# Performance work log

Hardware: AMD Instinct MI355X
Metric: run time of the kernel (lower is better)

The kernel has to match this reference:

```python
import jax, jax.numpy as jnp
import numpy as np

H = 4096        # hidden_size
NH = 32         # num query heads
NKV = 8         # num kv heads
D = H // NH     # head_dim = 128
S = 2048        # num tokens (single causal sequence)
THETA = 1000000.0
SCALE = D ** -0.5


def _rope(x, positions):
    # neox-style (rotate-half) RoPE over full head_dim, as vLLM's get_rope default
    half = D // 2
    inv_freq = 1.0 / (THETA ** (jnp.arange(half, dtype=jnp.float32) / half))
    ang = positions.astype(jnp.float32)[:, None] * inv_freq          # [S, D/2]
    cos = jnp.cos(ang)[:, None, :]                                   # [S, 1, D/2]
    sin = jnp.sin(ang)[:, None, :]
    x1, x2 = x[..., :half], x[..., half:]
    return jnp.concatenate([x1 * cos - x2 * sin, x2 * cos + x1 * sin], axis=-1)


def setup_inputs() -> dict:
    key = jax.random.key(0)
    k1, k2, k3 = jax.random.split(key, 3)
    positions = jnp.arange(S, dtype=jnp.int32)
    hidden_states = jax.random.normal(k1, (S, H), dtype=jnp.float32)
    w_qkv = jax.random.normal(k2, ((NH + 2 * NKV) * D, H), dtype=jnp.float32) * 0.02
    w_o = jax.random.normal(k3, (H, NH * D), dtype=jnp.float32) * 0.02
    return {"positions": positions, "hidden_states": hidden_states,
            "w_qkv": w_qkv, "w_o": w_o}


def reference(positions, hidden_states, w_qkv, w_o):
    # fused QKV projection (Linear, bias=False): x @ W^T
    qkv = hidden_states @ w_qkv.T                                    # [S, (NH+2*NKV)*D]
    q, k, v = jnp.split(qkv, [NH * D, (NH + NKV) * D], axis=-1)
    q = q.reshape(S, NH, D)
    k = k.reshape(S, NKV, D)
    v = v.reshape(S, NKV, D)
    # RoPE on q and k
    q = _rope(q, positions)
    k = _rope(k, positions)
    # GQA causal attention: group NH query heads onto NKV kv heads
    g = NH // NKV
    qg = q.reshape(S, NKV, g, D)
    scores = jnp.einsum('qhgd,khd->hgqk', qg, k) * SCALE             # [NKV, g, S, S]
    causal = positions[:, None] >= positions[None, :]                # [S, S]
    scores = jnp.where(causal[None, None], scores, jnp.float32(-1e30))
    probs = jax.nn.softmax(scores, axis=-1)
    o = jnp.einsum('hgqk,khd->qhgd', probs, v).reshape(S, NH * D)
    return o @ w_o.T                                                 # [S, H]
```

## Files before the change

kernel.cpp:

```cpp
#include <hip/hip_runtime.h>
#include <hip/hip_bf16.h>

#define S_LEN 2048
#define HID 4096
#define NH 32
#define NKV 8
#define DH 128
#define QKV_N ((NH + 2 * NKV) * DH)
#define SCALE_ATT 0.08838834764831845f
#define SCALE2_ATT 0.12751744f

typedef __bf16 bf16;
typedef __bf16 bf16x8 __attribute__((ext_vector_type(8)));
typedef __bf16 bf16x4 __attribute__((ext_vector_type(4)));
typedef float f32x4 __attribute__((ext_vector_type(4)));
typedef float f32x16 __attribute__((ext_vector_type(16)));

__device__ inline f32x4 mfma16(bf16x8 a, bf16x8 b, f32x4 c) {
    return __builtin_amdgcn_mfma_f32_16x16x32_bf16(a, b, c, 0, 0, 0);
}
__device__ inline f32x16 mfma32(bf16x8 a, bf16x8 b, f32x16 c) {
    return __builtin_amdgcn_mfma_f32_32x32x16_bf16(a, b, c, 0, 0, 0);
}

__device__ inline bf16x8 load8(const float* p) {
    const float4 a = ((const float4*)p)[0];
    const float4 b = ((const float4*)p)[1];
    bf16x8 r;
    r[0] = (bf16)a.x; r[1] = (bf16)a.y; r[2] = (bf16)a.z; r[3] = (bf16)a.w;
    r[4] = (bf16)b.x; r[5] = (bf16)b.y; r[6] = (bf16)b.z; r[7] = (bf16)b.w;
    return r;
}
__device__ inline bf16x8 load8(const bf16* p) { return *(const bf16x8*)p; }

__device__ inline void load_lds16(const bf16* g, bf16* lds_base) {
    __builtin_amdgcn_global_load_lds(
        (const __attribute__((address_space(1))) void*)g,
        (__attribute__((address_space(3))) void*)lds_base, 16, 0, 0);
}

__device__ inline unsigned pack2_bf16(float lo, float hi) {
    union { bf16 h[2]; unsigned u; } r;
    r.h[0] = (bf16)lo;
    r.h[1] = (bf16)hi;
    return r.u;
}

__global__ __launch_bounds__(256) void cvt3_kernel(const float* __restrict__ s0, bf16* __restrict__ d0, int c0,
                                                   const float* __restrict__ s1, bf16* __restrict__ d1, int c1,
                                                   const float* __restrict__ s2, bf16* __restrict__ d2, int c2) {
    int i = blockIdx.x * 256 + threadIdx.x;
    if (i < c0) { *(bf16x8*)&d0[(size_t)i * 8] = load8(&s0[(size_t)i * 8]); return; }
    i -= c0;
    if (i < c1) { *(bf16x8*)&d1[(size_t)i * 8] = load8(&s1[(size_t)i * 8]); return; }
    i -= c1;
    if (i < c2) { *(bf16x8*)&d2[(size_t)i * 8] = load8(&s2[(size_t)i * 8]); }
}

template <int BN, typename OutT>
__global__ __launch_bounds__(512, 2) void gemm_8ph(const bf16* __restrict__ A,
                                                   const bf16* __restrict__ B,
                                                   OutT* __restrict__ C,
                                                   int K, int lda, int ldc) {
    constexpr int WTN = BN / 4;
    constexpr int NREP = WTN / 32;
    extern __shared__ char smem[];
    bf16* As = (bf16*)smem;
    bf16* Bs = (bf16*)(smem + 2 * 256 * 64 * 2);

    const int tid = threadIdx.x;
    const int lane = tid & 63;
    const int w = tid >> 6;
    const int wm = w >> 2;
    const int wn = w & 3;
    const int ln = lane & 31;
    const int hi = lane >> 5;
    const int rseg = lane >> 3;
    const int gc = (lane & 7) ^ rseg;

    const int m0 = (int)blockIdx.y * 256;
    const int n0 = (int)blockIdx.x * BN;
    const int NT = K >> 6;

    auto stageA = [&](int pb, int kt, int h) {
        const int k0 = kt * 64;
        const int rb = h * 128 + w * 16;
        const bf16* src = &A[(size_t)(m0 + rb + rseg) * lda + k0 + gc * 8];
        bf16* dst = &As[pb * (256 * 64) + rb * 64];
        load_lds16(src, dst);
        load_lds16(src + (size_t)8 * lda, dst + 8 * 64);
    };
    auto stageB = [&](int pb, int kt, int h) {
        const int k0 = kt * 64;
        if constexpr (BN == 256) {
            const int rb = h * 128 + w * 16;
            const bf16* src = &B[(size_t)(n0 + rb + rseg) * K + k0 + gc * 8];
            bf16* dst = &Bs[pb * (BN * 64) + rb * 64];
            load_lds16(src, dst);
            load_lds16(src + (size_t)8 * K, dst + 8 * 64);
        } else {
            const int rb = h * 64 + w * 8;
            const bf16* src = &B[(size_t)(n0 + rb + rseg) * K + k0 + gc * 8];
            bf16* dst = &Bs[pb * (BN * 64) + rb * 64];
            load_lds16(src, dst);
        }
    };

    f32x16 acc[4][NREP];
#pragma unroll
    for (int mi = 0; mi < 4; ++mi)
#pragma unroll
        for (int j = 0; j < NREP; ++j)
#pragma unroll
            for (int r = 0; r < 16; ++r) acc[mi][j][r] = 0.f;

    stageB(0, 0, 0); stageB(0, 0, 1);
    stageA(0, 0, 0); stageA(0, 0, 1);
    {
        const int k1 = NT > 1 ? 1 : 0;
        stageB(1, k1, 0); stageB(1, k1, 1);
    }
    if constexpr (BN == 256)
        asm volatile("s_waitcnt vmcnt(4)" ::: "memory");
    else
        asm volatile("s_waitcnt vmcnt(2)" ::: "memory");
    __builtin_amdgcn_s_barrier();

    int p = 0;
    for (int u = 0; u < NT; ++u, p ^= 1) {
        const bf16* Ab = &As[p * (256 * 64)];
        const bf16* Bb = &Bs[p * (BN * 64)];
        const int ktA = u + 1 < NT ? u + 1 : NT - 1;
        const int ktB = u + 2 < NT ? u + 2 : NT - 1;
        bf16x8 bfr[NREP][4];
#pragma unroll
        for (int q = 0; q < 4; ++q) {
            if (q == 0) {
#pragma unroll
                for (int j = 0; j < NREP; ++j)
#pragma unroll
                    for (int kk = 0; kk < 4; ++kk) {
                        const int n = wn * WTN + j * 32 + ln;
                        bfr[j][kk] = *(const bf16x8*)&Bb[n * 64 + (((2 * kk + hi) ^ (ln & 7)) * 8)];
                    }
            }
            bf16x8 af[4];
#pragma unroll
            for (int kk = 0; kk < 4; ++kk) {
                const int m = wm * 128 + q * 32 + ln;
                af[kk] = *(const bf16x8*)&Ab[m * 64 + (((2 * kk + hi) ^ (ln & 7)) * 8)];
            }
            if (q == 0) stageA(p ^ 1, ktA, 0);
            else if (q == 1) stageA(p ^ 1, ktA, 1);
            else if (q == 2) stageB(p, ktB, 0);
            else stageB(p, ktB, 1);

            __builtin_amdgcn_s_barrier();
            asm volatile("s_waitcnt lgkmcnt(0)" ::: "memory");
            __builtin_amdgcn_sched_barrier(0);
            __builtin_amdgcn_s_setprio(1);
#pragma unroll
            for (int j = 0; j < NREP; ++j)
#pragma unroll
                for (int kk = 0; kk < 4; ++kk)
                    acc[q][j] = mfma32(af[kk], bfr[j][kk], acc[q][j]);
            __builtin_amdgcn_s_setprio(0);
            __builtin_amdgcn_sched_barrier(0);
            if (q == 3) {
                if constexpr (BN == 256)
                    asm volatile("s_waitcnt vmcnt(4)" ::: "memory");
                else
                    asm volatile("s_waitcnt vmcnt(2)" ::: "memory");
            }
            __builtin_amdgcn_s_barrier();
        }
    }
    asm volatile("s_waitcnt vmcnt(0)" ::: "memory");

#pragma unroll
    for (int mi = 0; mi < 4; ++mi)
#pragma unroll
        for (int j = 0; j < NREP; ++j)
#pragma unroll
            for (int r = 0; r < 16; ++r) {
                int row = m0 + wm * 128 + mi * 32 + (r & 3) + 8 * (r >> 2) + 4 * hi;
                int col = n0 + wn * WTN + j * 32 + ln;
                C[(size_t)row * ldc + col] = (OutT)acc[mi][j][r];
            }
}

template <typename AT, typename OutT>
__global__ __launch_bounds__(256) void gemm_bt(const AT* __restrict__ A,
                                               const float* __restrict__ B,
                                               OutT* __restrict__ C,
                                               int K, int lda, int ldc) {
    const int tid = threadIdx.x;
    const int lane = tid & 63;
    const int w = tid >> 6;
    const int m0 = blockIdx.y * 128;
    const int n0 = blockIdx.x * 128;
    const int wm = (w >> 1) * 64;
    const int wn = (w & 1) * 64;
    const int ln = lane & 15;
    const int qo = lane >> 4;

    __shared__ bf16 As[128 * 72];
    __shared__ bf16 Bs[128 * 72];

    f32x4 acc[4][4];
#pragma unroll
    for (int mi = 0; mi < 4; ++mi)
#pragma unroll
        for (int ni = 0; ni < 4; ++ni) acc[mi][ni] = f32x4{0.f, 0.f, 0.f, 0.f};

    for (int k0 = 0; k0 < K; k0 += 64) {
#pragma unroll
        for (int i = 0; i < 4; ++i) {
            int v = tid + i * 256;
            int row = v >> 3;
            int col = (v & 7) * 8;
            *(bf16x8*)&As[row * 72 + col] = load8(&A[(size_t)(m0 + row) * lda + k0 + col]);
            *(bf16x8*)&Bs[row * 72 + col] = load8(&B[(size_t)(n0 + row) * K + k0 + col]);
        }
        __syncthreads();
#pragma unroll
        for (int kk = 0; kk < 64; kk += 32) {
            bf16x8 af[4], bfr[4];
#pragma unroll
            for (int mi = 0; mi < 4; ++mi)
                af[mi] = *(const bf16x8*)&As[(wm + mi * 16 + ln) * 72 + kk + qo * 8];
#pragma unroll
            for (int ni = 0; ni < 4; ++ni)
                bfr[ni] = *(const bf16x8*)&Bs[(wn + ni * 16 + ln) * 72 + kk + qo * 8];
#pragma unroll
            for (int mi = 0; mi < 4; ++mi)
#pragma unroll
                for (int ni = 0; ni < 4; ++ni)
                    acc[mi][ni] = mfma16(af[mi], bfr[ni], acc[mi][ni]);
        }
        __syncthreads();
    }
#pragma unroll
    for (int mi = 0; mi < 4; ++mi)
#pragma unroll
        for (int ni = 0; ni < 4; ++ni)
#pragma unroll
            for (int r = 0; r < 4; ++r) {
                int row = m0 + wm + mi * 16 + qo * 4 + r;
                int col = n0 + wn + ni * 16 + ln;
                C[(size_t)row * ldc + col] = (OutT)acc[mi][ni][r];
            }
}

__global__ __launch_bounds__(256) void rope_kernel(bf16* __restrict__ qkv,
                                                   const int* __restrict__ positions) {
    int idx = blockIdx.x * 256 + threadIdx.x;
    const int total = S_LEN * (NH + NKV) * 64;
    if (idx >= total) return;
    int d = idx & 63;
    int t = idx >> 6;
    int head = t % (NH + NKV);
    int s = t / (NH + NKV);
    size_t base = (size_t)s * QKV_N + (head < NH ? head * DH : NH * DH + (head - NH) * DH);
    float x1 = (float)qkv[base + d];
    float x2 = (float)qkv[base + d + 64];
    float pos = (float)positions[s];
    float inv = expf(-0.21586735246819178f * (float)d);
    float ang = pos * inv;
    float c = cosf(ang);
    float sn = sinf(ang);
    qkv[base + d] = (bf16)(x1 * c - x2 * sn);
    qkv[base + d + 64] = (bf16)(x2 * c + x1 * sn);
}

__global__ __launch_bounds__(256) void vtrans_kernel(const bf16* __restrict__ qkv,
                                                     bf16* __restrict__ vt_g) {
    const int tid = threadIdx.x;
    const int s0 = blockIdx.x * 64;
    const int kvh = blockIdx.y;
    __shared__ bf16 Ls[64 * 136];
#pragma unroll
    for (int i = 0; i < 4; ++i) {
        int v = tid + i * 256;
        int row = v >> 4;
        int col = (v & 15) * 8;
        *(bf16x8*)&Ls[row * 136 + col] =
            *(const bf16x8*)&qkv[(size_t)(s0 + row) * QKV_N + (NH + NKV) * DH + kvh * DH + col];
    }
    __syncthreads();
#pragma unroll
    for (int i = 0; i < 4; ++i) {
        int u = tid + i * 256;
        int d = u >> 3;
        int sg = (u & 7) * 8;
        bf16x8 r;
#pragma unroll
        for (int j = 0; j < 8; ++j) r[j] = Ls[(sg + j) * 136 + d];
        *(bf16x8*)&vt_g[((size_t)kvh * DH + d) * S_LEN + s0 + sg] = r;
    }
}

__global__ __launch_bounds__(256) void attn_kernel(bf16* __restrict__ qkv,
                                                   const bf16* __restrict__ vt_g) {
    const int tid = threadIdx.x;
    const int lane = tid & 63;
    const int w = tid >> 6;
    const int ln = lane & 31;
    const int hi = lane >> 5;
    const int hq = blockIdx.x;
    const int qtile = (int)gridDim.y - 1 - (int)blockIdx.y;
    const int kvh = hq >> 2;
    const int q0 = qtile * 128;
    const int qrow = q0 + w * 32 + ln;

    __shared__ __align__(128) bf16 Ks[2][64 * 128];
    __shared__ __align__(128) bf16 Vt[2][128 * 64];

    bf16x8 qf[8];
    {
        const bf16* qptr = qkv + (size_t)qrow * QKV_N + hq * DH + hi * 8;
#pragma unroll
        for (int s = 0; s < 8; ++s) qf[s] = *(const bf16x8*)(qptr + s * 16);
    }

    const bf16* ksrc = qkv + NH * DH + kvh * DH;
    const bf16* vsrc = vt_g + (size_t)kvh * DH * S_LEN;
    const int kcK = lane & 15;
    const int krs = lane >> 4;
    const int kcV = lane & 7;
    const int vrs = lane >> 3;

    auto stage = [&](int buf, int kt) {
        const int k0s = kt * 64;
#pragma unroll
        for (int j = 0; j < 4; ++j) {
            int r = w * 16 + j * 4 + krs;
            load_lds16(ksrc + (size_t)(k0s + r) * QKV_N + ((kcK ^ (r & 7)) * 8),
                       &Ks[buf][(w * 16 + j * 4) * 128]);
        }
#pragma unroll
        for (int j = 0; j < 4; ++j) {
            int d = w * 32 + j * 8 + vrs;
            load_lds16(vsrc + (size_t)d * S_LEN + k0s + ((kcV ^ (d & 7)) * 8),
                       &Vt[buf][(w * 32 + j * 8) * 64]);
        }
    };

    f32x16 acc[4];
#pragma unroll
    for (int t = 0; t < 4; ++t)
#pragma unroll
        for (int r = 0; r < 16; ++r) acc[t][r] = 0.f;
    float m2 = -1e30f, l = 0.f;

    const int kt_last = (q0 + 127) >> 6;
    int buf = 0;
    stage(0, 0);
    __syncthreads();

    for (int kt = 0; kt <= kt_last; ++kt) {
        if (kt < kt_last) stage(buf ^ 1, kt + 1);
        const int k0 = kt * 64;
        if (k0 <= q0 + w * 32 + 31) {
            f32x16 st[2];
#pragma unroll
            for (int t = 0; t < 2; ++t)
#pragma unroll
                for (int r = 0; r < 16; ++r) st[t][r] = 0.f;
            const bf16* Kb = &Ks[buf][0];
            __builtin_amdgcn_s_setprio(1);
#pragma unroll
            for (int t = 0; t < 2; ++t) {
                const int key = t * 32 + ln;
#pragma unroll
                for (int s = 0; s < 8; ++s) {
                    bf16x8 kf =
                        *(const bf16x8*)&Kb[key * 128 + (((2 * s + hi) ^ (key & 7)) * 8)];
                    st[t] = mfma32(kf, qf[s], st[t]);
                }
            }
            __builtin_amdgcn_s_setprio(0);
            const bool needMask = (k0 + 63 > q0 + w * 32);
            float tmax = -1e30f;
#pragma unroll
            for (int t = 0; t < 2; ++t)
#pragma unroll
                for (int r = 0; r < 16; ++r) {
                    int kcol = k0 + t * 32 + (r & 3) + 8 * (r >> 2) + 4 * hi;
                    float v = st[t][r] * SCALE2_ATT;
                    if (needMask && kcol > qrow) v = -1e30f;
                    st[t][r] = v;
                    tmax = fmaxf(tmax, v);
                }
            tmax = fmaxf(tmax, __shfl_xor(tmax, 32, 64));
            float mnew = fmaxf(m2, tmax);
            float alpha = exp2f(m2 - mnew);
            float rs = 0.f;
#pragma unroll
            for (int t = 0; t < 2; ++t)
#pragma unroll
                for (int r = 0; r < 16; ++r) {
                    float e = exp2f(st[t][r] - mnew);
                    st[t][r] = e;
                    rs += e;
                }
            rs += __shfl_xor(rs, 32, 64);
            l = l * alpha + rs;
            m2 = mnew;
#pragma unroll
            for (int t = 0; t < 4; ++t)
#pragma unroll
                for (int r = 0; r < 16; ++r) acc[t][r] *= alpha;
            unsigned cw[16];
#pragma unroll
            for (int i = 0; i < 16; ++i)
                cw[i] = pack2_bf16(st[i >> 3][2 * (i & 7)], st[i >> 3][2 * (i & 7) + 1]);
            bf16x8 pa[4];
#pragma unroll
            for (int ks = 0; ks < 4; ++ks) {
                const int base = (ks >> 1) * 8 + (ks & 1) * 4;
                union { unsigned u[4]; bf16x8 v; } pk;
#pragma unroll
                for (int e = 0; e < 2; ++e) {
                    unsigned A = cw[base + e];
                    unsigned B = cw[base + 2 + e];
                    unsigned tA = (unsigned)__shfl_xor((int)A, 32, 64);
                    unsigned tB = (unsigned)__shfl_xor((int)B, 32, 64);
                    pk.u[e] = hi ? tB : A;
                    pk.u[e + 2] = hi ? B : tA;
                }
                pa[ks] = pk.v;
            }
            const bf16* Vb = &Vt[buf][0];
            __builtin_amdgcn_s_setprio(1);
#pragma unroll
            for (int dt = 0; dt < 4; ++dt) {
                const int d = dt * 32 + ln;
#pragma unroll
                for (int ks = 0; ks < 4; ++ks) {
                    bf16x8 vf =
                        *(const bf16x8*)&Vb[d * 64 + (((2 * ks + hi) ^ (d & 7)) * 8)];
                    acc[dt] = mfma32(vf, pa[ks], acc[dt]);
                }
            }
            __builtin_amdgcn_s_setprio(0);
        }
        __syncthreads();
        buf ^= 1;
    }

    const float invl = 1.f / l;
    bf16* outp = qkv + (size_t)qrow * QKV_N + hq * DH;
#pragma unroll
    for (int dt = 0; dt < 4; ++dt)
#pragma unroll
        for (int rq = 0; rq < 4; ++rq) {
            bf16x4 o;
#pragma unroll
            for (int i = 0; i < 4; ++i) o[i] = (bf16)(acc[dt][rq * 4 + i] * invl);
            *(bf16x4*)(outp + dt * 32 + rq * 8 + hi * 4) = o;
        }
}

extern "C" void kernel_launch(void* const* d_in, const int* in_sizes, int n_in,
                              void* d_out, int out_size, void* d_ws, size_t ws_size,
                              hipStream_t stream) {
    const int* positions = (const int*)d_in[0];
    const float* hidden = (const float*)d_in[1];
    const float* w_qkv = (const float*)d_in[2];
    const float* w_o = (const float*)d_in[3];
    float* out = (float*)d_out;

    const size_t n_qkv = (size_t)S_LEN * QKV_N;
    const size_t n_vt = (size_t)NKV * DH * S_LEN;
    const size_t n_hid = (size_t)S_LEN * HID;
    const size_t n_wqkv = (size_t)QKV_N * HID;
    const size_t n_wo = (size_t)HID * HID;

    const size_t need_min = (n_qkv + n_vt) * sizeof(bf16);
    const size_t need_full = (n_qkv + n_vt + n_hid + n_wqkv + n_wo) * sizeof(bf16);
    if (ws_size < need_min) return;

    bf16* qkv = (bf16*)d_ws;
    bf16* vt_g = qkv + n_qkv;
    bf16* hid_b = vt_g + n_vt;
    bf16* wqkv_b = hid_b + n_hid;
    bf16* wo_b = wqkv_b + n_wqkv;
    const bool full = ws_size >= need_full;

    if (full) {
        const int c0 = (int)(n_hid / 8), c1 = (int)(n_wqkv / 8), c2 = (int)(n_wo / 8);
        cvt3_kernel<<<(c0 + c1 + c2 + 255) / 256, 256, 0, stream>>>(hidden, hid_b, c0,
                                                                    w_qkv, wqkv_b, c1,
                                                                    w_o, wo_b, c2);
        hipFuncSetAttribute(reinterpret_cast<const void*>(&gemm_8ph<256, bf16>),
                            hipFuncAttributeMaxDynamicSharedMemorySize, 131072);
        gemm_8ph<256, bf16><<<dim3(QKV_N / 256, S_LEN / 256), 512, 131072, stream>>>(
            hid_b, wqkv_b, qkv, HID, HID, QKV_N);
    } else {
        gemm_bt<<<dim3(QKV_N / 128, S_LEN / 128), 256, 0, stream>>>(hidden, w_qkv, qkv, HID, HID, QKV_N);
    }
    const int total = S_LEN * (NH + NKV) * 64;
    rope_kernel<<<(total + 255) / 256, 256, 0, stream>>>(qkv, positions);
    vtrans_kernel<<<dim3(S_LEN / 64, NKV), 256, 0, stream>>>(qkv, vt_g);
    attn_kernel<<<dim3(NH, S_LEN / 128), 256, 0, stream>>>(qkv, vt_g);
    if (full) {
        hipFuncSetAttribute(reinterpret_cast<const void*>(&gemm_8ph<128, float>),
                            hipFuncAttributeMaxDynamicSharedMemorySize, 98304);
        gemm_8ph<128, float><<<dim3(HID / 128, S_LEN / 256), 512, 98304, stream>>>(
            qkv, wo_b, out, HID, QKV_N, HID);
    } else {
        gemm_bt<<<dim3(HID / 128, S_LEN / 128), 256, 0, stream>>>(qkv, w_o, out, HID, QKV_N, HID);
    }
}
```

Measured before the change: 537.2 us.

## Trim GEMM barriers, reuse RoPE sincos across heads, lazily rescale softmax

Three unrelated changes. The GEMM main loop drops two of its per-subtile barriers and keeps one at q==2 and one at the end of each k-tile. The RoPE kernel computes sincos once per (token, d) and loops over all 40 heads, so the transcendental work is no longer repeated per head. The attention kernel skips the running-max update and accumulator rescale when a wave's new max exceeds the old one by at most 11.5 in log2 space. That lazy rescale lets exponentials grow up to about 2^11.5 before rescaling, which bf16 P and fp32 accumulators should tolerate. The barrier removal risks LDS races if the stage and read ordering is not actually safe.

```diff
diff --git a/kernel.cpp b/kernel.cpp
--- a/kernel.cpp
+++ b/kernel.cpp
@@ -135,6 +135,7 @@
         bf16x8 bfr[NREP][4];
 #pragma unroll
         for (int q = 0; q < 4; ++q) {
+            if (q == 2) __builtin_amdgcn_s_barrier();
             if (q == 0) {
 #pragma unroll
                 for (int j = 0; j < NREP; ++j)
@@ -155,7 +156,6 @@
             else if (q == 2) stageB(p, ktB, 0);
             else stageB(p, ktB, 1);
 
-            __builtin_amdgcn_s_barrier();
             asm volatile("s_waitcnt lgkmcnt(0)" ::: "memory");
             __builtin_amdgcn_sched_barrier(0);
             __builtin_amdgcn_s_setprio(1);
@@ -171,8 +171,8 @@
                     asm volatile("s_waitcnt vmcnt(4)" ::: "memory");
                 else
                     asm volatile("s_waitcnt vmcnt(2)" ::: "memory");
-            }
-            __builtin_amdgcn_s_barrier();
+                __builtin_amdgcn_s_barrier();
+            }
         }
     }
     asm volatile("s_waitcnt vmcnt(0)" ::: "memory");
@@ -255,22 +255,23 @@
 __global__ __launch_bounds__(256) void rope_kernel(bf16* __restrict__ qkv,
                                                    const int* __restrict__ positions) {
     int idx = blockIdx.x * 256 + threadIdx.x;
-    const int total = S_LEN * (NH + NKV) * 64;
-    if (idx >= total) return;
+    if (idx >= S_LEN * 64) return;
     int d = idx & 63;
-    int t = idx >> 6;
-    int head = t % (NH + NKV);
-    int s = t / (NH + NKV);
-    size_t base = (size_t)s * QKV_N + (head < NH ? head * DH : NH * DH + (head - NH) * DH);
-    float x1 = (float)qkv[base + d];
-    float x2 = (float)qkv[base + d + 64];
+    int s = idx >> 6;
     float pos = (float)positions[s];
     float inv = expf(-0.21586735246819178f * (float)d);
     float ang = pos * inv;
-    float c = cosf(ang);
-    float sn = sinf(ang);
-    qkv[base + d] = (bf16)(x1 * c - x2 * sn);
-    qkv[base + d + 64] = (bf16)(x2 * c + x1 * sn);
+    float sn, c;
+    sincosf(ang, &sn, &c);
+    const size_t row = (size_t)s * QKV_N;
+#pragma unroll 8
+    for (int h = 0; h < NH + NKV; ++h) {
+        size_t base = row + (size_t)h * DH;
+        float x1 = (float)qkv[base + d];
+        float x2 = (float)qkv[base + d + 64];
+        qkv[base + d] = (bf16)(x1 * c - x2 * sn);
+        qkv[base + d + 64] = (bf16)(x2 * c + x1 * sn);
+    }
 }
 
 __global__ __launch_bounds__(256) void vtrans_kernel(const bf16* __restrict__ qkv,
@@ -393,8 +394,10 @@
                     tmax = fmaxf(tmax, v);
                 }
             tmax = fmaxf(tmax, __shfl_xor(tmax, 32, 64));
-            float mnew = fmaxf(m2, tmax);
-            float alpha = exp2f(m2 - mnew);
+            const bool skip = __all(tmax - m2 <= 11.5f);
+            float mnew, alpha;
+            if (skip) { mnew = m2; alpha = 1.f; }
+            else { mnew = fmaxf(m2, tmax); alpha = exp2f(m2 - mnew); }
             float rs = 0.f;
 #pragma unroll
             for (int t = 0; t < 2; ++t)
@@ -407,10 +410,12 @@
             rs += __shfl_xor(rs, 32, 64);
             l = l * alpha + rs;
             m2 = mnew;
-#pragma unroll
-            for (int t = 0; t < 4; ++t)
-#pragma unroll
-                for (int r = 0; r < 16; ++r) acc[t][r] *= alpha;
+            if (!skip) {
+#pragma unroll
+                for (int t = 0; t < 4; ++t)
+#pragma unroll
+                    for (int r = 0; r < 16; ++r) acc[t][r] *= alpha;
+            }
             unsigned cw[16];
 #pragma unroll
             for (int i = 0; i < 16; ++i)
@@ -500,8 +505,7 @@
     } else {
         gemm_bt<<<dim3(QKV_N / 128, S_LEN / 128), 256, 0, stream>>>(hidden, w_qkv, qkv, HID, HID, QKV_N);
     }
-    const int total = S_LEN * (NH + NKV) * 64;
-    rope_kernel<<<(total + 255) / 256, 256, 0, stream>>>(qkv, positions);
+    rope_kernel<<<(S_LEN * 64 + 255) / 256, 256, 0, stream>>>(qkv, positions);
     vtrans_kernel<<<dim3(S_LEN / 64, NKV), 256, 0, stream>>>(qkv, vt_g);
     attn_kernel<<<dim3(NH, S_LEN / 128), 256, 0, stream>>>(qkv, vt_g);
     if (full) {
```

After: 538.0 us. Within noise of the previous version (+0.2%).
